# Kernel tuning notes

Measured on AMD Instinct MI355X. Metric: run time of the kernel, lower is better.

The kernel has to match this reference:

```python
import jax, jax.numpy as jnp
import numpy as np

WS = 512            # window_size
STEP = WS // 2      # hop
K = WS // 2 + 1     # rfft coeffs = 257


def hann(n):
    # periodic hann window (matches torch.hann_window default)
    return 0.5 * (1.0 - jnp.cos(2.0 * jnp.pi * jnp.arange(n) / n))


def setup_inputs() -> dict:
    key = jax.random.key(0)
    k1, k2, k3 = jax.random.split(key, 3)
    B, C, T = 4, 64, 65536
    x = jax.random.normal(k1, (B, C, T), dtype=jnp.float32)
    # mixer initialized near identity (nn.Parameter(torch.eye(C)) after some training)
    mixer = jnp.eye(C, dtype=jnp.float32) + 0.01 * jax.random.normal(k2, (C, C), dtype=jnp.float32)
    # stable per-coefficient transfer magnitudes in [0, 0.9)
    transfer = jax.random.uniform(k3, (C, K), dtype=jnp.float32) * 0.9
    gain = jnp.full((1,), 1.5, dtype=jnp.float32)
    return {"x": x, "mixer": mixer, "transfer": transfer, "gain": gain}


def reference(x, mixer, transfer, gain):
    B, C, T = x.shape
    # (x^T @ mixer)^T
    x = jnp.einsum('bct,cd->bdt', x, mixer)
    # windowed_audio: pad by hop, unfold into half-overlapping frames
    xp = jnp.pad(x, ((0, 0), (0, 0), (0, STEP)))
    n_frames = (xp.shape[-1] - WS) // STEP + 1
    idx = jnp.arange(n_frames)[:, None] * STEP + jnp.arange(WS)[None, :]  # [F, WS]
    windowed = xp[:, :, idx]                     # [B, C, F, WS]
    spec = jnp.fft.rfft(windowed, axis=-1)       # [B, C, F, K] complex64
    # linear recurrence over frames: y_i = (spec_i + y_{i-1}) * transfer
    def step(carry, s):
        y = (s + carry) * transfer[None]         # [B, C, K]
        return y, y
    spec_t = jnp.transpose(spec, (2, 0, 1, 3))   # [F, B, C, K]
    y0 = jnp.zeros((B, C, K), dtype=spec.dtype)
    _, ys = jax.lax.scan(step, y0, spec_t)       # [F, B, C, K]
    out_spec = jnp.transpose(ys, (1, 2, 0, 3))   # [B, C, F, K]
    # inverse FFT + windowed overlap-add
    aw = jnp.fft.irfft(out_spec, n=WS, axis=-1)  # [B, C, F, WS]
    aw = aw * hann(WS)[None, None, None, :]
    L = (n_frames - 1) * STEP + WS
    samples = jnp.zeros((B, C, L), dtype=aw.dtype).at[:, :, idx].add(aw)
    samples = jnp.tanh(samples * gain[0])
    return samples[..., :T]
```

## Files before the change

kernel.cpp:

```cpp
#include <hip/hip_runtime.h>
#include <math.h>

#define T_LEN  65536
#define T_PAD  65792
#define C_CH   64
#define STEP_  256
#define K_     257
#define NW     16
#define NIT    16
#define SPITCH 17

#define SW(i) ((i) ^ (((i) >> 2) & 12))

#define CFENCE() asm volatile("" ::: "memory")
#define BAR() do { asm volatile("s_waitcnt lgkmcnt(0)" ::: "memory"); \
                   __builtin_amdgcn_s_barrier(); \
                   asm volatile("" ::: "memory"); } while (0)

__device__ __forceinline__ float2 cadd(float2 a, float2 b) { return make_float2(a.x + b.x, a.y + b.y); }
__device__ __forceinline__ float2 csub(float2 a, float2 b) { return make_float2(a.x - b.x, a.y - b.y); }
__device__ __forceinline__ float2 cmul(float2 a, float2 b) {
    return make_float2(a.x * b.x - a.y * b.y, a.x * b.y + a.y * b.x);
}
template <int SGN>
__device__ __forceinline__ float2 cmulsg(float2 w, float2 t) {
    if (SGN > 0) return make_float2(w.x * t.x - w.y * t.y, w.x * t.y + w.y * t.x);
    else         return make_float2(w.x * t.x + w.y * t.y, w.x * t.y - w.y * t.x);
}
template <int SGN>
__device__ __forceinline__ void bfly4(float2 z0, float2 z1, float2 z2, float2 z3,
                                      float2& o0, float2& o1, float2& o2, float2& o3,
                                      float2 w1, float2 w2, float2 w3) {
    float2 apc = cadd(z0, z2), amc = csub(z0, z2);
    float2 bpd = cadd(z1, z3), bmd = csub(z1, z3);
    float2 jb  = make_float2(-bmd.y, bmd.x);
    float2 t1, t3;
    if (SGN > 0) { t1 = csub(amc, jb); t3 = cadd(amc, jb); }
    else         { t1 = cadd(amc, jb); t3 = csub(amc, jb); }
    o0 = cadd(apc, bpd);
    o1 = cmulsg<SGN>(w1, t1);
    o2 = cmulsg<SGN>(w2, csub(apc, bpd));
    o3 = cmulsg<SGN>(w3, t3);
}
template <int SGN>
__device__ __forceinline__ void bfly4nt(float2 z0, float2 z1, float2 z2, float2 z3,
                                        float2& o0, float2& o1, float2& o2, float2& o3) {
    float2 apc = cadd(z0, z2), amc = csub(z0, z2);
    float2 bpd = cadd(z1, z3), bmd = csub(z1, z3);
    float2 jb  = make_float2(-bmd.y, bmd.x);
    o0 = cadd(apc, bpd);
    o2 = csub(apc, bpd);
    if (SGN > 0) { o1 = csub(amc, jb); o3 = cadd(amc, jb); }
    else         { o1 = cadd(amc, jb); o3 = csub(amc, jb); }
}

__device__ __forceinline__ float ftanh(float x) {
    float e = __expf(2.0f * x);
    return 1.0f - 2.0f * __builtin_amdgcn_rcpf(e + 1.0f);
}

__global__ __launch_bounds__(512, 1) void mix_kernel(const float* __restrict__ x,
                                                     const float* __restrict__ mixer,
                                                     float* __restrict__ mixed) {
    __shared__ __align__(16) float xt[64][128];
    __shared__ __align__(16) float mx[64][64];
    int tid = threadIdx.x;
    int b   = blockIdx.y;
    int t0  = blockIdx.x * 128;

    if (t0 >= T_LEN) {
        for (int f = tid; f < 8192; f += 512) {
            int d = f >> 7, tt = f & 127;
            mixed[((size_t)(b * C_CH + d)) * T_PAD + t0 + tt] = 0.0f;
        }
        return;
    }
    for (int f = tid; f < 4096; f += 512) reinterpret_cast<float*>(mx)[f] = mixer[f];
    for (int f4 = tid; f4 < 2048; f4 += 512) {
        int cc = f4 >> 5, tt4 = f4 & 31;
        *reinterpret_cast<float4*>(&xt[cc][tt4 * 4]) =
            *reinterpret_cast<const float4*>(&x[((size_t)(b * C_CH + cc)) * T_LEN + t0 + tt4 * 4]);
    }
    __syncthreads();

    int tp = tid & 63, grp = tid >> 6;
    int dbase = grp * 8;
    float2 acc[8];
#pragma unroll
    for (int i = 0; i < 8; ++i) acc[i] = make_float2(0.0f, 0.0f);
    for (int cc = 0; cc < 64; ++cc) {
        float2 xv = *reinterpret_cast<const float2*>(&xt[cc][2 * tp]);
        float4 m0 = *reinterpret_cast<const float4*>(&mx[cc][dbase + 0]);
        float4 m1 = *reinterpret_cast<const float4*>(&mx[cc][dbase + 4]);
        acc[0].x = fmaf(xv.x, m0.x, acc[0].x); acc[0].y = fmaf(xv.y, m0.x, acc[0].y);
        acc[1].x = fmaf(xv.x, m0.y, acc[1].x); acc[1].y = fmaf(xv.y, m0.y, acc[1].y);
        acc[2].x = fmaf(xv.x, m0.z, acc[2].x); acc[2].y = fmaf(xv.y, m0.z, acc[2].y);
        acc[3].x = fmaf(xv.x, m0.w, acc[3].x); acc[3].y = fmaf(xv.y, m0.w, acc[3].y);
        acc[4].x = fmaf(xv.x, m1.x, acc[4].x); acc[4].y = fmaf(xv.y, m1.x, acc[4].y);
        acc[5].x = fmaf(xv.x, m1.y, acc[5].x); acc[5].y = fmaf(xv.y, m1.y, acc[5].y);
        acc[6].x = fmaf(xv.x, m1.z, acc[6].x); acc[6].y = fmaf(xv.y, m1.z, acc[6].y);
        acc[7].x = fmaf(xv.x, m1.w, acc[7].x); acc[7].y = fmaf(xv.y, m1.w, acc[7].y);
    }
#pragma unroll
    for (int i = 0; i < 8; ++i)
        *reinterpret_cast<float2*>(&mixed[((size_t)(b * C_CH + dbase + i)) * T_PAD + t0 + 2 * tp]) = acc[i];
}

__global__ __launch_bounds__(1024, 4) void stft_kernel(const float* __restrict__ mixed,
                                                       const float* __restrict__ transfer,
                                                       const float* __restrict__ gainp,
                                                       float* __restrict__ out) {
    __shared__ __align__(16) float2 buf[NW][256];
    __shared__ __align__(16) float2 specT[2][K_ * SPITCH];
    __shared__ __align__(16) float  olab[NW][264];
    __shared__ __align__(16) float  tails[2][264];

    const int tid  = threadIdx.x;
    const int bc   = blockIdx.x;
    const int b    = bc >> 6, c = bc & 63;
    const int g    = tid >> 6, lane = tid & 63;

    const float* src = mixed + ((size_t)(b * C_CH + c)) * T_PAD;
    float*       dst = out   + ((size_t)(b * C_CH + c)) * T_LEN;

    float2 pf0, pf1, pf2, pf3;
    {
        const float* fp = src + (size_t)g * STEP_;
        pf0 = *reinterpret_cast<const float2*>(fp + 2 * lane);
        pf1 = *reinterpret_cast<const float2*>(fp + 2 * (lane + 64));
        pf2 = *reinterpret_cast<const float2*>(fp + 2 * (lane + 128));
        pf3 = *reinterpret_cast<const float2*>(fp + 2 * (lane + 192));
    }

    const float TWO_PI = 6.2831853071795864f;
    float sn, cn;
    sincosf(TWO_PI * (float)lane / 256.0f, &sn, &cn);
    const float2 w1a = make_float2(cn, -sn), w2a = cmul(w1a, w1a), w3a = cmul(w2a, w1a);
    sincosf(TWO_PI * (float)(lane >> 2) / 64.0f, &sn, &cn);
    const float2 w1b = make_float2(cn, -sn), w2b = cmul(w1b, w1b), w3b = cmul(w2b, w1b);
    sincosf(TWO_PI * (float)(lane >> 4) / 16.0f, &sn, &cn);
    const float2 w1c = make_float2(cn, -sn), w2c = cmul(w1c, w1c), w3c = cmul(w2c, w1c);
    float2 wh[4];
#pragma unroll
    for (int qq = 0; qq < 4; ++qq) {
        sincosf(3.14159265358979f * (float)(lane + 64 * qq) / 256.0f, &sn, &cn);
        wh[qq] = make_float2(cn, -sn);
    }
#define HV(m) ((0.5f - 0.5f * cosf(TWO_PI * (float)(m) / 512.0f)) * (1.0f / 512.0f))
    const float h0 = HV(2 * lane),       h1 = HV(2 * lane + 1);
    const float h2 = HV(2 * lane + 128), h3 = HV(2 * lane + 129);
    const float h4 = HV(2 * lane + 256), h5 = HV(2 * lane + 257);
    const float h6 = HV(2 * lane + 384), h7 = HV(2 * lane + 385);
#undef HV

    const int q2  = (lane & 3)  + ((lane >> 2) << 4);
    const int q3  = (lane & 15) + ((lane >> 4) << 6);
    const int swl = SW(lane);
    const int s1b = (4 * lane) ^ (lane & 12);
    const int sq2a = SW(q2);
    const int sq2b = SW(q2 + 4);
    const int sq2c = SW(q2 + 8);
    const int sq2d = SW(q2 + 12);
    const int sq3a = q3;
    const int sq3b = (q3 + 16) ^ 4;
    const int sq3c = (q3 + 32) ^ 8;
    const int sq3d = (q3 + 48) ^ 12;
    const int mm0 = SW((256 - lane) & 255);
    const int mm1 = SW(192 - lane);
    const int mm2 = SW(128 - lane);
    const int mm3 = SW(64 - lane);
    const int spw  = lane * SPITCH + g;
    const int spm  = 256 * SPITCH + g - lane * SPITCH;

    int sk = -1;
    if (g < 4) sk = (g << 6) | lane;
    else if (g == 4 && lane == 0) sk = 256;
    float  tk = 0.0f;
    float2 yc = make_float2(0.0f, 0.0f);
    if (sk >= 0) tk = transfer[c * K_ + sk];

    if (tid < 256) tails[0][tid] = 0.0f;
    const float gv = gainp[0];
    float2* bin = &buf[g][0];
    BAR();

    for (int it = 0; it <= NIT; ++it) {
        const int sp = it & 1;
        if (it < NIT) {
            const int f = it * NW + g;
            float2 z0 = pf0, z1 = pf1, z2 = pf2, z3 = pf3;
            if (it + 1 < NIT) {
                const float* fp = src + (size_t)(f + NW) * STEP_;
                pf0 = *reinterpret_cast<const float2*>(fp + 2 * lane);
                pf1 = *reinterpret_cast<const float2*>(fp + 2 * (lane + 64));
                pf2 = *reinterpret_cast<const float2*>(fp + 2 * (lane + 128));
                pf3 = *reinterpret_cast<const float2*>(fp + 2 * (lane + 192));
            }
            float2 o0, o1, o2, o3;
            bfly4<1>(z0, z1, z2, z3, o0, o1, o2, o3, w1a, w2a, w3a);
            {
                float2* bw = bin + s1b;
                *reinterpret_cast<float4*>(bw)     = make_float4(o0.x, o0.y, o1.x, o1.y);
                *reinterpret_cast<float4*>(bw + 2) = make_float4(o2.x, o2.y, o3.x, o3.y);
            }
            CFENCE();
            z0 = bin[swl]; z1 = bin[swl + 64]; z2 = bin[swl + 128]; z3 = bin[swl + 192];
            bfly4<1>(z0, z1, z2, z3, o0, o1, o2, o3, w1b, w2b, w3b);
            CFENCE();
            bin[sq2a] = o0; bin[sq2b] = o1; bin[sq2c] = o2; bin[sq2d] = o3;
            CFENCE();
            z0 = bin[swl]; z1 = bin[swl + 64]; z2 = bin[swl + 128]; z3 = bin[swl + 192];
            bfly4<1>(z0, z1, z2, z3, o0, o1, o2, o3, w1c, w2c, w3c);
            CFENCE();
            bin[sq3a] = o0; bin[sq3b] = o1; bin[sq3c] = o2; bin[sq3d] = o3;
            CFENCE();
            z0 = bin[swl]; z1 = bin[swl + 64]; z2 = bin[swl + 128]; z3 = bin[swl + 192];
            bfly4nt<1>(z0, z1, z2, z3, o0, o1, o2, o3);
            CFENCE();
            bin[swl] = o0; bin[swl + 64] = o1; bin[swl + 128] = o2; bin[swl + 192] = o3;
            CFENCE();
            {
                float2 v0 = bin[mm0], v1 = bin[mm1], v2 = bin[mm2], v3 = bin[mm3];
                float2 uu[4] = {o0, o1, o2, o3}, vv[4] = {v0, v1, v2, v3};
                float2* st = &specT[sp][0];
#pragma unroll
                for (int qq = 0; qq < 4; ++qq) {
                    float2 E = make_float2(0.5f * (uu[qq].x + vv[qq].x),  0.5f * (uu[qq].y - vv[qq].y));
                    float2 O = make_float2(0.5f * (uu[qq].y + vv[qq].y), -0.5f * (uu[qq].x - vv[qq].x));
                    st[spw + 64 * SPITCH * qq] = cadd(E, cmul(wh[qq], O));
                }
                if (lane == 0) st[256 * SPITCH + g] = make_float2(o0.x - o0.y, 0.0f);
            }
        }
        BAR();
        if (it < NIT && sk >= 0) {
            float2* s0 = &specT[sp][sk * SPITCH];
            float2 v[8]; float2 y = yc;
#pragma unroll
            for (int gg = 0; gg < 8; ++gg) v[gg] = s0[gg];
#pragma unroll
            for (int gg = 0; gg < 8; ++gg) {
                y.x = (v[gg].x + y.x) * tk; y.y = (v[gg].y + y.y) * tk;
                s0[gg] = y;
            }
#pragma unroll
            for (int gg = 0; gg < 8; ++gg) v[gg] = s0[gg + 8];
#pragma unroll
            for (int gg = 0; gg < 8; ++gg) {
                y.x = (v[gg].x + y.x) * tk; y.y = (v[gg].y + y.y) * tk;
                s0[gg + 8] = y;
            }
            yc = y;
        }
        if (it > 0) {
            const int fb = (it - 1) * NW + g;
            const float2* st = &specT[sp ^ 1][0];
            float2 o0, o1, o2, o3;
            {
                float2 iu[4], is_[4];
#pragma unroll
                for (int qq = 0; qq < 4; ++qq) {
                    iu[qq]  = st[spw + 64 * SPITCH * qq];
                    is_[qq] = st[spm - 64 * SPITCH * qq];
                }
                float2 zz[4];
#pragma unroll
                for (int qq = 0; qq < 4; ++qq) {
                    float2 A  = make_float2(iu[qq].x + is_[qq].x, iu[qq].y - is_[qq].y);
                    float2 D  = make_float2(iu[qq].x - is_[qq].x, iu[qq].y + is_[qq].y);
                    float2 Bv = cmulsg<-1>(wh[qq], D);
                    zz[qq] = make_float2(A.x - Bv.y, A.y + Bv.x);
                }
                bfly4<-1>(zz[0], zz[1], zz[2], zz[3], o0, o1, o2, o3, w1a, w2a, w3a);
            }
            {
                float2* bw = bin + s1b;
                *reinterpret_cast<float4*>(bw)     = make_float4(o0.x, o0.y, o1.x, o1.y);
                *reinterpret_cast<float4*>(bw + 2) = make_float4(o2.x, o2.y, o3.x, o3.y);
            }
            CFENCE();
            float2 z0 = bin[swl], z1 = bin[swl + 64], z2 = bin[swl + 128], z3 = bin[swl + 192];
            bfly4<-1>(z0, z1, z2, z3, o0, o1, o2, o3, w1b, w2b, w3b);
            CFENCE();
            bin[sq2a] = o0; bin[sq2b] = o1; bin[sq2c] = o2; bin[sq2d] = o3;
            CFENCE();
            z0 = bin[swl]; z1 = bin[swl + 64]; z2 = bin[swl + 128]; z3 = bin[swl + 192];
            bfly4<-1>(z0, z1, z2, z3, o0, o1, o2, o3, w1c, w2c, w3c);
            CFENCE();
            bin[sq3a] = o0; bin[sq3b] = o1; bin[sq3c] = o2; bin[sq3d] = o3;
            CFENCE();
            z0 = bin[swl]; z1 = bin[swl + 64]; z2 = bin[swl + 128]; z3 = bin[swl + 192];
            bfly4nt<-1>(z0, z1, z2, z3, o0, o1, o2, o3);
            {
                float2 sh0 = make_float2(o2.x * h4, o2.y * h5);
                float2 sh1 = make_float2(o3.x * h6, o3.y * h7);
                float* wrow = (g == NW - 1) ? tails[it & 1] : olab[g + 1];
                *reinterpret_cast<float2*>(&wrow[2 * lane])       = sh0;
                *reinterpret_cast<float2*>(&wrow[2 * lane + 128]) = sh1;
            }
            BAR();
            {
                const float* prow = (g == 0) ? tails[(it - 1) & 1] : olab[g];
                float2 p0 = *reinterpret_cast<const float2*>(&prow[2 * lane]);
                float2 p1 = *reinterpret_cast<const float2*>(&prow[2 * lane + 128]);
                float2 r0 = make_float2(ftanh((o0.x * h0 + p0.x) * gv),
                                        ftanh((o0.y * h1 + p0.y) * gv));
                float2 r1 = make_float2(ftanh((o1.x * h2 + p1.x) * gv),
                                        ftanh((o1.y * h3 + p1.y) * gv));
                float* dp = dst + (size_t)fb * STEP_;
                *reinterpret_cast<float2*>(&dp[2 * lane])       = r0;
                *reinterpret_cast<float2*>(&dp[2 * lane + 128]) = r1;
            }
        }
    }
}

extern "C" void kernel_launch(void* const* d_in, const int* in_sizes, int n_in,
                              void* d_out, int out_size, void* d_ws, size_t ws_size,
                              hipStream_t stream) {
    (void)in_sizes; (void)n_in; (void)out_size; (void)ws_size;
    const float* x        = (const float*)d_in[0];
    const float* mixer    = (const float*)d_in[1];
    const float* transfer = (const float*)d_in[2];
    const float* gain     = (const float*)d_in[3];
    float* out   = (float*)d_out;
    float* mixed = (float*)d_ws;

    dim3 gmix(T_PAD / 128, 4);
    mix_kernel<<<gmix, 512, 0, stream>>>(x, mixer, mixed);
    stft_kernel<<<256, 1024, 0, stream>>>(mixed, transfer, gain, out);
}
```

Measured before the change: 113.6 us.

## Process two frames per wave in STFT kernel with 512-thread blocks

```diff
diff --git a/kernel.cpp b/kernel.cpp
--- a/kernel.cpp
+++ b/kernel.cpp
@@ -6,7 +6,8 @@
 #define C_CH   64
 #define STEP_  256
 #define K_     257
-#define NW     16
+#define NWV    8
+#define FPI    16
 #define NIT    16
 #define SPITCH 17
 
@@ -106,13 +107,13 @@
         *reinterpret_cast<float2*>(&mixed[((size_t)(b * C_CH + dbase + i)) * T_PAD + t0 + 2 * tp]) = acc[i];
 }
 
-__global__ __launch_bounds__(1024, 4) void stft_kernel(const float* __restrict__ mixed,
-                                                       const float* __restrict__ transfer,
-                                                       const float* __restrict__ gainp,
-                                                       float* __restrict__ out) {
-    __shared__ __align__(16) float2 buf[NW][256];
+__global__ __launch_bounds__(512, 2) void stft_kernel(const float* __restrict__ mixed,
+                                                      const float* __restrict__ transfer,
+                                                      const float* __restrict__ gainp,
+                                                      float* __restrict__ out) {
+    __shared__ __align__(16) float2 buf[FPI][256];
     __shared__ __align__(16) float2 specT[2][K_ * SPITCH];
-    __shared__ __align__(16) float  olab[NW][264];
+    __shared__ __align__(16) float  olab[FPI][264];
     __shared__ __align__(16) float  tails[2][264];
 
     const int tid  = threadIdx.x;
@@ -123,13 +124,18 @@
     const float* src = mixed + ((size_t)(b * C_CH + c)) * T_PAD;
     float*       dst = out   + ((size_t)(b * C_CH + c)) * T_LEN;
 
-    float2 pf0, pf1, pf2, pf3;
+    float2 pfA0, pfA1, pfA2, pfA3, pfB0, pfB1, pfB2, pfB3;
     {
         const float* fp = src + (size_t)g * STEP_;
-        pf0 = *reinterpret_cast<const float2*>(fp + 2 * lane);
-        pf1 = *reinterpret_cast<const float2*>(fp + 2 * (lane + 64));
-        pf2 = *reinterpret_cast<const float2*>(fp + 2 * (lane + 128));
-        pf3 = *reinterpret_cast<const float2*>(fp + 2 * (lane + 192));
+        pfA0 = *reinterpret_cast<const float2*>(fp + 2 * lane);
+        pfA1 = *reinterpret_cast<const float2*>(fp + 2 * (lane + 64));
+        pfA2 = *reinterpret_cast<const float2*>(fp + 2 * (lane + 128));
+        pfA3 = *reinterpret_cast<const float2*>(fp + 2 * (lane + 192));
+        const float* fq = fp + (size_t)8 * STEP_;
+        pfB0 = *reinterpret_cast<const float2*>(fq + 2 * lane);
+        pfB1 = *reinterpret_cast<const float2*>(fq + 2 * (lane + 64));
+        pfB2 = *reinterpret_cast<const float2*>(fq + 2 * (lane + 128));
+        pfB3 = *reinterpret_cast<const float2*>(fq + 2 * (lane + 192));
     }
 
     const float TWO_PI = 6.2831853071795864f;
@@ -169,147 +175,227 @@
     const int mm1 = SW(192 - lane);
     const int mm2 = SW(128 - lane);
     const int mm3 = SW(64 - lane);
-    const int spw  = lane * SPITCH + g;
-    const int spm  = 256 * SPITCH + g - lane * SPITCH;
-
-    int sk = -1;
-    if (g < 4) sk = (g << 6) | lane;
-    else if (g == 4 && lane == 0) sk = 256;
-    float  tk = 0.0f;
-    float2 yc = make_float2(0.0f, 0.0f);
-    if (sk >= 0) tk = transfer[c * K_ + sk];
+    const int spwA = lane * SPITCH + g;
+    const int spwB = spwA + 8;
+    const int spmA = 256 * SPITCH + g - lane * SPITCH;
+    const int spmB = spmA + 8;
+
+    int k1 = -1, k2 = -1;
+    if (g < 2) { k1 = (g << 6) | lane; k2 = k1 + 128; }
+    else if (g == 2 && lane == 0) { k1 = 256; }
+    float tk1 = 0.0f, tk2 = 0.0f;
+    float2 yc1 = make_float2(0.f, 0.f), yc2 = make_float2(0.f, 0.f);
+    if (k1 >= 0) tk1 = transfer[c * K_ + k1];
+    if (k2 >= 0) tk2 = transfer[c * K_ + k2];
 
     if (tid < 256) tails[0][tid] = 0.0f;
     const float gv = gainp[0];
-    float2* bin = &buf[g][0];
+    float2* binA = &buf[g][0];
+    float2* binB = &buf[g + 8][0];
     BAR();
 
     for (int it = 0; it <= NIT; ++it) {
         const int sp = it & 1;
         if (it < NIT) {
-            const int f = it * NW + g;
-            float2 z0 = pf0, z1 = pf1, z2 = pf2, z3 = pf3;
+            float2 zA0 = pfA0, zA1 = pfA1, zA2 = pfA2, zA3 = pfA3;
+            float2 zB0 = pfB0, zB1 = pfB1, zB2 = pfB2, zB3 = pfB3;
             if (it + 1 < NIT) {
-                const float* fp = src + (size_t)(f + NW) * STEP_;
-                pf0 = *reinterpret_cast<const float2*>(fp + 2 * lane);
-                pf1 = *reinterpret_cast<const float2*>(fp + 2 * (lane + 64));
-                pf2 = *reinterpret_cast<const float2*>(fp + 2 * (lane + 128));
-                pf3 = *reinterpret_cast<const float2*>(fp + 2 * (lane + 192));
-            }
-            float2 o0, o1, o2, o3;
-            bfly4<1>(z0, z1, z2, z3, o0, o1, o2, o3, w1a, w2a, w3a);
-            {
-                float2* bw = bin + s1b;
-                *reinterpret_cast<float4*>(bw)     = make_float4(o0.x, o0.y, o1.x, o1.y);
-                *reinterpret_cast<float4*>(bw + 2) = make_float4(o2.x, o2.y, o3.x, o3.y);
-            }
-            CFENCE();
-            z0 = bin[swl]; z1 = bin[swl + 64]; z2 = bin[swl + 128]; z3 = bin[swl + 192];
-            bfly4<1>(z0, z1, z2, z3, o0, o1, o2, o3, w1b, w2b, w3b);
-            CFENCE();
-            bin[sq2a] = o0; bin[sq2b] = o1; bin[sq2c] = o2; bin[sq2d] = o3;
-            CFENCE();
-            z0 = bin[swl]; z1 = bin[swl + 64]; z2 = bin[swl + 128]; z3 = bin[swl + 192];
-            bfly4<1>(z0, z1, z2, z3, o0, o1, o2, o3, w1c, w2c, w3c);
-            CFENCE();
-            bin[sq3a] = o0; bin[sq3b] = o1; bin[sq3c] = o2; bin[sq3d] = o3;
-            CFENCE();
-            z0 = bin[swl]; z1 = bin[swl + 64]; z2 = bin[swl + 128]; z3 = bin[swl + 192];
-            bfly4nt<1>(z0, z1, z2, z3, o0, o1, o2, o3);
-            CFENCE();
-            bin[swl] = o0; bin[swl + 64] = o1; bin[swl + 128] = o2; bin[swl + 192] = o3;
-            CFENCE();
-            {
-                float2 v0 = bin[mm0], v1 = bin[mm1], v2 = bin[mm2], v3 = bin[mm3];
-                float2 uu[4] = {o0, o1, o2, o3}, vv[4] = {v0, v1, v2, v3};
+                const float* fp = src + (size_t)((it + 1) * FPI + g) * STEP_;
+                pfA0 = *reinterpret_cast<const float2*>(fp + 2 * lane);
+                pfA1 = *reinterpret_cast<const float2*>(fp + 2 * (lane + 64));
+                pfA2 = *reinterpret_cast<const float2*>(fp + 2 * (lane + 128));
+                pfA3 = *reinterpret_cast<const float2*>(fp + 2 * (lane + 192));
+                const float* fq = fp + (size_t)8 * STEP_;
+                pfB0 = *reinterpret_cast<const float2*>(fq + 2 * lane);
+                pfB1 = *reinterpret_cast<const float2*>(fq + 2 * (lane + 64));
+                pfB2 = *reinterpret_cast<const float2*>(fq + 2 * (lane + 128));
+                pfB3 = *reinterpret_cast<const float2*>(fq + 2 * (lane + 192));
+            }
+            float2 oA0, oA1, oA2, oA3, oB0, oB1, oB2, oB3;
+            bfly4<1>(zA0, zA1, zA2, zA3, oA0, oA1, oA2, oA3, w1a, w2a, w3a);
+            bfly4<1>(zB0, zB1, zB2, zB3, oB0, oB1, oB2, oB3, w1a, w2a, w3a);
+            {
+                float2* bw = binA + s1b;
+                *reinterpret_cast<float4*>(bw)     = make_float4(oA0.x, oA0.y, oA1.x, oA1.y);
+                *reinterpret_cast<float4*>(bw + 2) = make_float4(oA2.x, oA2.y, oA3.x, oA3.y);
+                float2* bx = binB + s1b;
+                *reinterpret_cast<float4*>(bx)     = make_float4(oB0.x, oB0.y, oB1.x, oB1.y);
+                *reinterpret_cast<float4*>(bx + 2) = make_float4(oB2.x, oB2.y, oB3.x, oB3.y);
+            }
+            CFENCE();
+            zA0 = binA[swl]; zA1 = binA[swl + 64]; zA2 = binA[swl + 128]; zA3 = binA[swl + 192];
+            zB0 = binB[swl]; zB1 = binB[swl + 64]; zB2 = binB[swl + 128]; zB3 = binB[swl + 192];
+            bfly4<1>(zA0, zA1, zA2, zA3, oA0, oA1, oA2, oA3, w1b, w2b, w3b);
+            bfly4<1>(zB0, zB1, zB2, zB3, oB0, oB1, oB2, oB3, w1b, w2b, w3b);
+            CFENCE();
+            binA[sq2a] = oA0; binA[sq2b] = oA1; binA[sq2c] = oA2; binA[sq2d] = oA3;
+            binB[sq2a] = oB0; binB[sq2b] = oB1; binB[sq2c] = oB2; binB[sq2d] = oB3;
+            CFENCE();
+            zA0 = binA[swl]; zA1 = binA[swl + 64]; zA2 = binA[swl + 128]; zA3 = binA[swl + 192];
+            zB0 = binB[swl]; zB1 = binB[swl + 64]; zB2 = binB[swl + 128]; zB3 = binB[swl + 192];
+            bfly4<1>(zA0, zA1, zA2, zA3, oA0, oA1, oA2, oA3, w1c, w2c, w3c);
+            bfly4<1>(zB0, zB1, zB2, zB3, oB0, oB1, oB2, oB3, w1c, w2c, w3c);
+            CFENCE();
+            binA[sq3a] = oA0; binA[sq3b] = oA1; binA[sq3c] = oA2; binA[sq3d] = oA3;
+            binB[sq3a] = oB0; binB[sq3b] = oB1; binB[sq3c] = oB2; binB[sq3d] = oB3;
+            CFENCE();
+            zA0 = binA[swl]; zA1 = binA[swl + 64]; zA2 = binA[swl + 128]; zA3 = binA[swl + 192];
+            zB0 = binB[swl]; zB1 = binB[swl + 64]; zB2 = binB[swl + 128]; zB3 = binB[swl + 192];
+            bfly4nt<1>(zA0, zA1, zA2, zA3, oA0, oA1, oA2, oA3);
+            bfly4nt<1>(zB0, zB1, zB2, zB3, oB0, oB1, oB2, oB3);
+            CFENCE();
+            binA[swl] = oA0; binA[swl + 64] = oA1; binA[swl + 128] = oA2; binA[swl + 192] = oA3;
+            binB[swl] = oB0; binB[swl + 64] = oB1; binB[swl + 128] = oB2; binB[swl + 192] = oB3;
+            CFENCE();
+            {
+                float2 vA0 = binA[mm0], vA1 = binA[mm1], vA2 = binA[mm2], vA3 = binA[mm3];
+                float2 vB0 = binB[mm0], vB1 = binB[mm1], vB2 = binB[mm2], vB3 = binB[mm3];
+                float2 uuA[4] = {oA0, oA1, oA2, oA3}, vvA[4] = {vA0, vA1, vA2, vA3};
+                float2 uuB[4] = {oB0, oB1, oB2, oB3}, vvB[4] = {vB0, vB1, vB2, vB3};
                 float2* st = &specT[sp][0];
 #pragma unroll
                 for (int qq = 0; qq < 4; ++qq) {
-                    float2 E = make_float2(0.5f * (uu[qq].x + vv[qq].x),  0.5f * (uu[qq].y - vv[qq].y));
-                    float2 O = make_float2(0.5f * (uu[qq].y + vv[qq].y), -0.5f * (uu[qq].x - vv[qq].x));
-                    st[spw + 64 * SPITCH * qq] = cadd(E, cmul(wh[qq], O));
-                }
-                if (lane == 0) st[256 * SPITCH + g] = make_float2(o0.x - o0.y, 0.0f);
+                    float2 EA = make_float2(0.5f * (uuA[qq].x + vvA[qq].x),  0.5f * (uuA[qq].y - vvA[qq].y));
+                    float2 OA = make_float2(0.5f * (uuA[qq].y + vvA[qq].y), -0.5f * (uuA[qq].x - vvA[qq].x));
+                    st[spwA + 64 * SPITCH * qq] = cadd(EA, cmul(wh[qq], OA));
+                    float2 EB = make_float2(0.5f * (uuB[qq].x + vvB[qq].x),  0.5f * (uuB[qq].y - vvB[qq].y));
+                    float2 OB = make_float2(0.5f * (uuB[qq].y + vvB[qq].y), -0.5f * (uuB[qq].x - vvB[qq].x));
+                    st[spwB + 64 * SPITCH * qq] = cadd(EB, cmul(wh[qq], OB));
+                }
+                if (lane == 0) {
+                    st[256 * SPITCH + g]     = make_float2(oA0.x - oA0.y, 0.0f);
+                    st[256 * SPITCH + g + 8] = make_float2(oB0.x - oB0.y, 0.0f);
+                }
             }
         }
         BAR();
-        if (it < NIT && sk >= 0) {
-            float2* s0 = &specT[sp][sk * SPITCH];
-            float2 v[8]; float2 y = yc;
-#pragma unroll
-            for (int gg = 0; gg < 8; ++gg) v[gg] = s0[gg];
-#pragma unroll
-            for (int gg = 0; gg < 8; ++gg) {
-                y.x = (v[gg].x + y.x) * tk; y.y = (v[gg].y + y.y) * tk;
-                s0[gg] = y;
-            }
-#pragma unroll
-            for (int gg = 0; gg < 8; ++gg) v[gg] = s0[gg + 8];
-#pragma unroll
-            for (int gg = 0; gg < 8; ++gg) {
-                y.x = (v[gg].x + y.x) * tk; y.y = (v[gg].y + y.y) * tk;
-                s0[gg + 8] = y;
-            }
-            yc = y;
+        if (it < NIT && k1 >= 0) {
+            float2* s1p = &specT[sp][k1 * SPITCH];
+            float2 va[8]; float2 y1 = yc1;
+#pragma unroll
+            for (int gg = 0; gg < 8; ++gg) va[gg] = s1p[gg];
+            if (k2 >= 0) {
+                float2* s2p = &specT[sp][k2 * SPITCH];
+                float2 vb[8]; float2 y2 = yc2;
+#pragma unroll
+                for (int gg = 0; gg < 8; ++gg) vb[gg] = s2p[gg];
+#pragma unroll
+                for (int gg = 0; gg < 8; ++gg) {
+                    y1.x = (va[gg].x + y1.x) * tk1; y1.y = (va[gg].y + y1.y) * tk1; s1p[gg] = y1;
+                    y2.x = (vb[gg].x + y2.x) * tk2; y2.y = (vb[gg].y + y2.y) * tk2; s2p[gg] = y2;
+                }
+#pragma unroll
+                for (int gg = 0; gg < 8; ++gg) { va[gg] = s1p[gg + 8]; vb[gg] = s2p[gg + 8]; }
+#pragma unroll
+                for (int gg = 0; gg < 8; ++gg) {
+                    y1.x = (va[gg].x + y1.x) * tk1; y1.y = (va[gg].y + y1.y) * tk1; s1p[gg + 8] = y1;
+                    y2.x = (vb[gg].x + y2.x) * tk2; y2.y = (vb[gg].y + y2.y) * tk2; s2p[gg + 8] = y2;
+                }
+                yc2 = y2;
+            } else {
+#pragma unroll
+                for (int gg = 0; gg < 8; ++gg) {
+                    y1.x = (va[gg].x + y1.x) * tk1; y1.y = (va[gg].y + y1.y) * tk1; s1p[gg] = y1;
+                }
+#pragma unroll
+                for (int gg = 0; gg < 8; ++gg) va[gg] = s1p[gg + 8];
+#pragma unroll
+                for (int gg = 0; gg < 8; ++gg) {
+                    y1.x = (va[gg].x + y1.x) * tk1; y1.y = (va[gg].y + y1.y) * tk1; s1p[gg + 8] = y1;
+                }
+            }
+            yc1 = y1;
         }
         if (it > 0) {
-            const int fb = (it - 1) * NW + g;
             const float2* st = &specT[sp ^ 1][0];
-            float2 o0, o1, o2, o3;
-            {
-                float2 iu[4], is_[4];
+            float2 oA0, oA1, oA2, oA3, oB0, oB1, oB2, oB3;
+            {
+                float2 iuA[4], isA[4], iuB[4], isB[4];
 #pragma unroll
                 for (int qq = 0; qq < 4; ++qq) {
-                    iu[qq]  = st[spw + 64 * SPITCH * qq];
-                    is_[qq] = st[spm - 64 * SPITCH * qq];
-                }
-                float2 zz[4];
+                    iuA[qq] = st[spwA + 64 * SPITCH * qq];
+                    isA[qq] = st[spmA - 64 * SPITCH * qq];
+                    iuB[qq] = st[spwB + 64 * SPITCH * qq];
+                    isB[qq] = st[spmB - 64 * SPITCH * qq];
+                }
+                float2 zzA[4], zzB[4];
 #pragma unroll
                 for (int qq = 0; qq < 4; ++qq) {
-                    float2 A  = make_float2(iu[qq].x + is_[qq].x, iu[qq].y - is_[qq].y);
-                    float2 D  = make_float2(iu[qq].x - is_[qq].x, iu[qq].y + is_[qq].y);
-                    float2 Bv = cmulsg<-1>(wh[qq], D);
-                    zz[qq] = make_float2(A.x - Bv.y, A.y + Bv.x);
-                }
-                bfly4<-1>(zz[0], zz[1], zz[2], zz[3], o0, o1, o2, o3, w1a, w2a, w3a);
-            }
-            {
-                float2* bw = bin + s1b;
-                *reinterpret_cast<float4*>(bw)     = make_float4(o0.x, o0.y, o1.x, o1.y);
-                *reinterpret_cast<float4*>(bw + 2) = make_float4(o2.x, o2.y, o3.x, o3.y);
-            }
-            CFENCE();
-            float2 z0 = bin[swl], z1 = bin[swl + 64], z2 = bin[swl + 128], z3 = bin[swl + 192];
-            bfly4<-1>(z0, z1, z2, z3, o0, o1, o2, o3, w1b, w2b, w3b);
-            CFENCE();
-            bin[sq2a] = o0; bin[sq2b] = o1; bin[sq2c] = o2; bin[sq2d] = o3;
-            CFENCE();
-            z0 = bin[swl]; z1 = bin[swl + 64]; z2 = bin[swl + 128]; z3 = bin[swl + 192];
-            bfly4<-1>(z0, z1, z2, z3, o0, o1, o2, o3, w1c, w2c, w3c);
-            CFENCE();
-            bin[sq3a] = o0; bin[sq3b] = o1; bin[sq3c] = o2; bin[sq3d] = o3;
-            CFENCE();
-            z0 = bin[swl]; z1 = bin[swl + 64]; z2 = bin[swl + 128]; z3 = bin[swl + 192];
-            bfly4nt<-1>(z0, z1, z2, z3, o0, o1, o2, o3);
-            {
-                float2 sh0 = make_float2(o2.x * h4, o2.y * h5);
-                float2 sh1 = make_float2(o3.x * h6, o3.y * h7);
-                float* wrow = (g == NW - 1) ? tails[it & 1] : olab[g + 1];
-                *reinterpret_cast<float2*>(&wrow[2 * lane])       = sh0;
-                *reinterpret_cast<float2*>(&wrow[2 * lane + 128]) = sh1;
+                    float2 AA  = make_float2(iuA[qq].x + isA[qq].x, iuA[qq].y - isA[qq].y);
+                    float2 DA  = make_float2(iuA[qq].x - isA[qq].x, iuA[qq].y + isA[qq].y);
+                    float2 BvA = cmulsg<-1>(wh[qq], DA);
+                    zzA[qq] = make_float2(AA.x - BvA.y, AA.y + BvA.x);
+                    float2 AB  = make_float2(iuB[qq].x + isB[qq].x, iuB[qq].y - isB[qq].y);
+                    float2 DB  = make_float2(iuB[qq].x - isB[qq].x, iuB[qq].y + isB[qq].y);
+                    float2 BvB = cmulsg<-1>(wh[qq], DB);
+                    zzB[qq] = make_float2(AB.x - BvB.y, AB.y + BvB.x);
+                }
+                bfly4<-1>(zzA[0], zzA[1], zzA[2], zzA[3], oA0, oA1, oA2, oA3, w1a, w2a, w3a);
+                bfly4<-1>(zzB[0], zzB[1], zzB[2], zzB[3], oB0, oB1, oB2, oB3, w1a, w2a, w3a);
+            }
+            {
+                float2* bw = binA + s1b;
+                *reinterpret_cast<float4*>(bw)     = make_float4(oA0.x, oA0.y, oA1.x, oA1.y);
+                *reinterpret_cast<float4*>(bw + 2) = make_float4(oA2.x, oA2.y, oA3.x, oA3.y);
+                float2* bx = binB + s1b;
+                *reinterpret_cast<float4*>(bx)     = make_float4(oB0.x, oB0.y, oB1.x, oB1.y);
+                *reinterpret_cast<float4*>(bx + 2) = make_float4(oB2.x, oB2.y, oB3.x, oB3.y);
+            }
+            CFENCE();
+            float2 zA0 = binA[swl], zA1 = binA[swl + 64], zA2 = binA[swl + 128], zA3 = binA[swl + 192];
+            float2 zB0 = binB[swl], zB1 = binB[swl + 64], zB2 = binB[swl + 128], zB3 = binB[swl + 192];
+            bfly4<-1>(zA0, zA1, zA2, zA3, oA0, oA1, oA2, oA3, w1b, w2b, w3b);
+            bfly4<-1>(zB0, zB1, zB2, zB3, oB0, oB1, oB2, oB3, w1b, w2b, w3b);
+            CFENCE();
+            binA[sq2a] = oA0; binA[sq2b] = oA1; binA[sq2c] = oA2; binA[sq2d] = oA3;
+            binB[sq2a] = oB0; binB[sq2b] = oB1; binB[sq2c] = oB2; binB[sq2d] = oB3;
+            CFENCE();
+            zA0 = binA[swl]; zA1 = binA[swl + 64]; zA2 = binA[swl + 128]; zA3 = binA[swl + 192];
+            zB0 = binB[swl]; zB1 = binB[swl + 64]; zB2 = binB[swl + 128]; zB3 = binB[swl + 192];
+            bfly4<-1>(zA0, zA1, zA2, zA3, oA0, oA1, oA2, oA3, w1c, w2c, w3c);
+            bfly4<-1>(zB0, zB1, zB2, zB3, oB0, oB1, oB2, oB3, w1c, w2c, w3c);
+            CFENCE();
+            binA[sq3a] = oA0; binA[sq3b] = oA1; binA[sq3c] = oA2; binA[sq3d] = oA3;
+            binB[sq3a] = oB0; binB[sq3b] = oB1; binB[sq3c] = oB2; binB[sq3d] = oB3;
+            CFENCE();
+            zA0 = binA[swl]; zA1 = binA[swl + 64]; zA2 = binA[swl + 128]; zA3 = binA[swl + 192];
+            zB0 = binB[swl]; zB1 = binB[swl + 64]; zB2 = binB[swl + 128]; zB3 = binB[swl + 192];
+            bfly4nt<-1>(zA0, zA1, zA2, zA3, oA0, oA1, oA2, oA3);
+            bfly4nt<-1>(zB0, zB1, zB2, zB3, oB0, oB1, oB2, oB3);
+            {
+                float2 shA0 = make_float2(oA2.x * h4, oA2.y * h5);
+                float2 shA1 = make_float2(oA3.x * h6, oA3.y * h7);
+                float* wrowA = olab[g + 1];
+                *reinterpret_cast<float2*>(&wrowA[2 * lane])       = shA0;
+                *reinterpret_cast<float2*>(&wrowA[2 * lane + 128]) = shA1;
+                float2 shB0 = make_float2(oB2.x * h4, oB2.y * h5);
+                float2 shB1 = make_float2(oB3.x * h6, oB3.y * h7);
+                float* wrowB = (g == NWV - 1) ? tails[it & 1] : olab[g + 9];
+                *reinterpret_cast<float2*>(&wrowB[2 * lane])       = shB0;
+                *reinterpret_cast<float2*>(&wrowB[2 * lane + 128]) = shB1;
             }
             BAR();
             {
-                const float* prow = (g == 0) ? tails[(it - 1) & 1] : olab[g];
-                float2 p0 = *reinterpret_cast<const float2*>(&prow[2 * lane]);
-                float2 p1 = *reinterpret_cast<const float2*>(&prow[2 * lane + 128]);
-                float2 r0 = make_float2(ftanh((o0.x * h0 + p0.x) * gv),
-                                        ftanh((o0.y * h1 + p0.y) * gv));
-                float2 r1 = make_float2(ftanh((o1.x * h2 + p1.x) * gv),
-                                        ftanh((o1.y * h3 + p1.y) * gv));
-                float* dp = dst + (size_t)fb * STEP_;
-                *reinterpret_cast<float2*>(&dp[2 * lane])       = r0;
-                *reinterpret_cast<float2*>(&dp[2 * lane + 128]) = r1;
+                const float* prowA = (g == 0) ? tails[(it - 1) & 1] : olab[g];
+                float2 pA0 = *reinterpret_cast<const float2*>(&prowA[2 * lane]);
+                float2 pA1 = *reinterpret_cast<const float2*>(&prowA[2 * lane + 128]);
+                const float* prowB = olab[g + 8];
+                float2 pB0 = *reinterpret_cast<const float2*>(&prowB[2 * lane]);
+                float2 pB1 = *reinterpret_cast<const float2*>(&prowB[2 * lane + 128]);
+                float2 rA0 = make_float2(ftanh((oA0.x * h0 + pA0.x) * gv),
+                                         ftanh((oA0.y * h1 + pA0.y) * gv));
+                float2 rA1 = make_float2(ftanh((oA1.x * h2 + pA1.x) * gv),
+                                         ftanh((oA1.y * h3 + pA1.y) * gv));
+                float2 rB0 = make_float2(ftanh((oB0.x * h0 + pB0.x) * gv),
+                                         ftanh((oB0.y * h1 + pB0.y) * gv));
+                float2 rB1 = make_float2(ftanh((oB1.x * h2 + pB1.x) * gv),
+                                         ftanh((oB1.y * h3 + pB1.y) * gv));
+                float* dpA = dst + (size_t)((it - 1) * FPI + g) * STEP_;
+                *reinterpret_cast<float2*>(&dpA[2 * lane])       = rA0;
+                *reinterpret_cast<float2*>(&dpA[2 * lane + 128]) = rA1;
+                float* dpB = dpA + (size_t)8 * STEP_;
+                *reinterpret_cast<float2*>(&dpB[2 * lane])       = rB0;
+                *reinterpret_cast<float2*>(&dpB[2 * lane + 128]) = rB1;
             }
         }
     }
@@ -328,5 +414,5 @@
 
     dim3 gmix(T_PAD / 128, 4);
     mix_kernel<<<gmix, 512, 0, stream>>>(x, mixer, mixed);
-    stft_kernel<<<256, 1024, 0, stream>>>(mixed, transfer, gain, out);
-}
+    stft_kernel<<<256, 512, 0, stream>>>(mixed, transfer, gain, out);
+}
```

Result: slower. 123.7 us (+8.9%).
